# Optimization experiments

Measured on AMD Instinct MI355X. Metric: run time of the kernel, lower is better.

Reference implementation:

```python
import jax, jax.numpy as jnp
import numpy as np

D = 2048
N = 4096
HEAD = 2
DH = D // HEAD


def setup_inputs() -> dict:
    key = jax.random.key(0)
    ks = jax.random.split(key, 7)
    s = 0.02  # realistic init scale for weights
    x = jax.random.normal(ks[0], (1, N, D), jnp.float32)
    Wq1 = jax.random.normal(ks[1], (DH, DH), jnp.float32) * s
    Wq2 = jax.random.normal(ks[2], (DH, DH), jnp.float32) * s
    Wk1 = jax.random.normal(ks[3], (DH, DH), jnp.float32) * s
    Wk2 = jax.random.normal(ks[4], (DH, DH), jnp.float32) * s
    Wv1 = jax.random.normal(ks[5], (DH, DH), jnp.float32) * s
    Wv2 = jax.random.normal(ks[6], (DH, DH), jnp.float32) * s
    return {"x": x, "Wq1": Wq1, "Wq2": Wq2, "Wk1": Wk1, "Wk2": Wk2,
            "Wv1": Wv1, "Wv2": Wv2}


def _head(xh, Wq, Wk, Wv):
    # xh: [1, N, Dh]; Linear applies in @ W^T (no bias)
    q = (xh @ Wq.T)[0]                      # [N, Dh]
    k = (xh @ Wk.T)[0]                      # [N, Dh] (k reshaped to 2D in torch)
    v = (xh @ Wv.T)[0]                      # [N, Dh]
    # QK_T linear with weight dynamically set to k (detached in torch):
    Sc = q @ jax.lax.stop_gradient(k).T     # [N, N]
    # Sc_V linear on v^T with weight set to Sc (detached in torch):
    Sc = jax.lax.stop_gradient(Sc)
    return v.T @ Sc.T                       # [Dh, N]  == (Sc @ v)^T


def reference(x, Wq1, Wq2, Wk1, Wk2, Wv1, Wv2):
    Dh = Wq1.shape[0]
    x1, x2 = x[..., :Dh], x[..., Dh:]       # torch.chunk(x, 2, dim=2)
    o1 = _head(x1, Wq1, Wk1, Wv1)           # [Dh, N]
    o2 = _head(x2, Wq2, Wk2, Wv2)           # [Dh, N]
    out = jnp.concatenate([o1, o2], axis=0).T  # transpose(-2,-1).squeeze -> [N, D]
    return out
```

## Files before the change

kernel.cpp:

```cpp
#include <hip/hip_runtime.h>
#include <hip/hip_bf16.h>


using bf16 = __hip_bfloat16;
typedef __attribute__((ext_vector_type(8))) __bf16 bf16x8;
typedef __attribute__((ext_vector_type(8))) unsigned short u16x8;
typedef __attribute__((ext_vector_type(4))) float f32x4;

#define M1 (1024 * 1024)

struct GB {
    const bf16* A[8];
    const bf16* B[8];
    void*       C[8];
    int lda[8];
    int ldb[8];
};

__device__ __forceinline__ void gload_lds16(const void* g, void* l) {
    __builtin_amdgcn_global_load_lds(
        (const __attribute__((address_space(1))) void*)g,
        (__attribute__((address_space(3))) void*)l, 16, 0, 0);
}

__device__ __forceinline__ void waitv0() {
    asm volatile("s_waitcnt vmcnt(0)" ::: "memory");
}

template<int BM_, int BN_, typename OUT_T>
__device__ __forceinline__ void gemm_core(
    const bf16* __restrict__ A, int lda,
    const bf16* __restrict__ B, int ldb,
    OUT_T* __restrict__ C, int ldc,
    int m0, int n0, int Ksub,
    unsigned short* smem, int tid)
{
    constexpr int BK = 64;
    unsigned short* As = smem;
    unsigned short* Bs = smem + BM_ * BK;

    constexpr int MI = BM_ / 32;
    constexpr int NI = BN_ / 32;

    const int lane = tid & 63;
    const int wave = tid >> 6;
    const int wm   = wave >> 1;
    const int wn   = wave & 1;
    const int fr = lane & 15;
    const int kg = lane >> 4;

    const int srow  = tid >> 3;
    const int scol  = (tid & 7) * 8;
    const int scolg = scol ^ ((srow & 7) << 3);

    f32x4 acc[MI][NI];
    #pragma unroll
    for (int i = 0; i < MI; ++i)
        #pragma unroll
        for (int j = 0; j < NI; ++j)
            acc[i][j] = {0.f, 0.f, 0.f, 0.f};

    const int niter = Ksub >> 6;
    for (int it = 0; it < niter; ++it) {
        const int kt = it << 6;
        #pragma unroll
        for (int r = 0; r < BM_ / 32; ++r)
            gload_lds16(A + (size_t)(m0 + r * 32 + srow) * lda + (kt + scolg),
                        &As[(r * 32 + srow) * BK + scol]);
        #pragma unroll
        for (int r = 0; r < BN_ / 32; ++r)
            gload_lds16(B + (size_t)(n0 + r * 32 + srow) * ldb + (kt + scolg),
                        &Bs[(r * 32 + srow) * BK + scol]);
        waitv0();
        __builtin_amdgcn_s_barrier();
        __builtin_amdgcn_sched_barrier(0);

        #pragma unroll
        for (int kk = 0; kk < 2; ++kk) {
            bf16x8 af[MI], bfg[NI];
            #pragma unroll
            for (int mi = 0; mi < MI; ++mi) {
                const int row = wm * (BM_ / 2) + mi * 16 + fr;
                const int c = (kk * 32 + kg * 8) ^ ((row & 7) << 3);
                af[mi] = *(const bf16x8*)&As[row * BK + c];
            }
            #pragma unroll
            for (int ni = 0; ni < NI; ++ni) {
                const int row = wn * (BN_ / 2) + ni * 16 + fr;
                const int c = (kk * 32 + kg * 8) ^ ((row & 7) << 3);
                bfg[ni] = *(const bf16x8*)&Bs[row * BK + c];
            }
            #pragma unroll
            for (int mi = 0; mi < MI; ++mi)
                #pragma unroll
                for (int ni = 0; ni < NI; ++ni)
                    acc[mi][ni] = __builtin_amdgcn_mfma_f32_16x16x32_bf16(
                        af[mi], bfg[ni], acc[mi][ni], 0, 0, 0);
        }

        __builtin_amdgcn_sched_barrier(0);
        __builtin_amdgcn_s_barrier();
        __builtin_amdgcn_sched_barrier(0);
    }

    if constexpr (sizeof(OUT_T) == 2) {
        #pragma unroll
        for (int mi = 0; mi < MI; ++mi)
            #pragma unroll
            for (int ni = 0; ni < NI; ++ni) {
                const int c = wn * (BN_ / 2) + ni * 16 + fr;
                #pragma unroll
                for (int j = 0; j < 4; ++j) {
                    const int r = wm * (BM_ / 2) + mi * 16 + kg * 4 + j;
                    bf16 h = __float2bfloat16(acc[mi][ni][j]);
                    smem[r * BN_ + c] = *(unsigned short*)&h;
                }
            }
        __syncthreads();
        constexpr int V = (BM_ * BN_) / 2048;
        #pragma unroll
        for (int v = 0; v < V; ++v) {
            const int off = v * 2048 + tid * 8;
            const int r = off / BN_;
            const int c = off % BN_;
            *(u16x8*)((unsigned short*)C + (size_t)(m0 + r) * ldc + n0 + c) =
                *(const u16x8*)&smem[off];
        }
    } else {
        float* fs = (float*)smem;
        #pragma unroll
        for (int mi = 0; mi < MI; ++mi)
            #pragma unroll
            for (int ni = 0; ni < NI; ++ni) {
                const int c = wn * (BN_ / 2) + ni * 16 + fr;
                #pragma unroll
                for (int j = 0; j < 4; ++j) {
                    const int r = wm * (BM_ / 2) + mi * 16 + kg * 4 + j;
                    fs[r * BN_ + c] = acc[mi][ni][j];
                }
            }
        __syncthreads();
        constexpr int V = (BM_ * BN_) / 1024;
        #pragma unroll
        for (int v = 0; v < V; ++v) {
            const int off = v * 1024 + tid * 4;
            const int r = off / BN_;
            const int c = off % BN_;
            *(float4*)((float*)C + (size_t)(m0 + r) * ldc + n0 + c) =
                *(const float4*)&fs[off];
        }
    }
}

template<int BM_, int BN_, typename OUT_T>
__global__ __launch_bounds__(256, 4)
void gemm_bt_pa(GB g, int Ksub, int ldc)
{
    constexpr int STAGE_SH = (BM_ + BN_) * 64;
    constexpr int EPI_SH   = BM_ * BN_ * (int)sizeof(OUT_T) / 2;
    constexpr int SMEM_SH  = STAGE_SH > EPI_SH ? STAGE_SH : EPI_SH;
    __shared__ __align__(16) unsigned short smem[SMEM_SH];

    const int gx = gridDim.x, gy = gridDim.y;
    const int nwg = gx * gy * gridDim.z;
    const int orig = blockIdx.x + gx * (blockIdx.y + gy * blockIdx.z);
    const int cpx = nwg >> 3;
    const int wg = (orig & 7) * cpx + (orig >> 3);
    const int bx = wg % gx;
    const int by = (wg / gx) % gy;
    const int bz = wg / (gx * gy);

    gemm_core<BM_, BN_, OUT_T>(g.A[bz], g.lda[bz], g.B[bz], g.ldb[bz],
                               (OUT_T*)g.C[bz], ldc,
                               by * BM_, bx * BN_, Ksub,
                               smem, threadIdx.x);
}

struct B1Args {
    const bf16* xt;
    const bf16* wdst;
    bf16* Gp;
    bf16* Mb;
};

__global__ __launch_bounds__(256, 4)
void b1_kernel(B1Args a)
{
    __shared__ __align__(16) unsigned short smem[16384];

    const int nwg = 704;
    const int orig = blockIdx.x;
    const int cpx = nwg >> 3;
    const int wg = (orig & 7) * cpx + (orig >> 3);

    if (wg < 576) {
        const int z = wg / 36;
        const int tile = wg - z * 36;
        const int h = z >> 3, s = z & 7;
        int ti = 0, rem = tile;
        while (rem >= 8 - ti) { rem -= 8 - ti; ++ti; }
        const int tj = ti + rem;
        const bf16* A = a.xt + (size_t)(h * 1024 + ti * 128) * 4096 + s * 512;
        const bf16* B = a.xt + (size_t)(h * 1024 + tj * 128) * 4096 + s * 512;
        bf16* C = a.Gp + ((size_t)z * 36 + tile) * 16384;
        gemm_core<128, 128, bf16>(A, 4096, B, 4096, C, 128, 0, 0, 512,
                                  smem, threadIdx.x);
    } else {
        const int idx = wg - 576;
        const int h = idx >> 6;
        const int tile = idx & 63;
        const int m0 = (tile >> 3) * 128;
        const int n0 = (tile & 7) * 128;
        const bf16* A = a.wdst + (size_t)h * M1;
        const bf16* B = a.wdst + (size_t)(2 + h) * M1;
        bf16* C = a.Mb + (size_t)h * M1;
        gemm_core<128, 128, bf16>(A, 1024, B, 1024, C, 1024, m0, n0, 1024,
                                  smem, threadIdx.x);
    }
}


__device__ __forceinline__ ushort4 cvt4(float4 v) {
    ushort4 o; bf16 h;
    h = __float2bfloat16(v.x); o.x = *(unsigned short*)&h;
    h = __float2bfloat16(v.y); o.y = *(unsigned short*)&h;
    h = __float2bfloat16(v.z); o.z = *(unsigned short*)&h;
    h = __float2bfloat16(v.w); o.w = *(unsigned short*)&h;
    return o;
}

struct PrepArgs {
    const float* x;
    const float* w[4];
    const float* wv[2];
    bf16* xb;
    bf16* xt;
    bf16* wdst;
};

__device__ void xpose64(const float* __restrict__ src, int ldsrc,
                        int r0, int c0,
                        bf16* __restrict__ dstS, int ldS,
                        bf16* __restrict__ dstT, int ldT,
                        float (*tile)[65], int t)
{
    const int tr  = t >> 4;
    const int tc4 = (t & 15) * 4;
    #pragma unroll
    for (int ph = 0; ph < 4; ++ph) {
        const int row = ph * 16 + tr;
        float4 v = *(const float4*)(src + (size_t)(r0 + row) * ldsrc + c0 + tc4);
        tile[row][tc4 + 0] = v.x;
        tile[row][tc4 + 1] = v.y;
        tile[row][tc4 + 2] = v.z;
        tile[row][tc4 + 3] = v.w;
        if (dstS)
            *(ushort4*)((unsigned short*)dstS + (size_t)(r0 + row) * ldS + c0 + tc4) = cvt4(v);
    }
    __syncthreads();
    #pragma unroll
    for (int ph = 0; ph < 4; ++ph) {
        const int crow = ph * 16 + tr;
        float4 v = {tile[tc4 + 0][crow], tile[tc4 + 1][crow],
                    tile[tc4 + 2][crow], tile[tc4 + 3][crow]};
        *(ushort4*)((unsigned short*)dstT + (size_t)(c0 + crow) * ldT + r0 + tc4) = cvt4(v);
    }
}

__global__ void prep(PrepArgs p)
{
    __shared__ float tile[64][65];
    const int b = blockIdx.x;
    const int t = threadIdx.x;

    if (b < 2048) {
        const int n0 = (b & 63) * 64;
        const int c0 = (b >> 6) * 64;
        xpose64(p.x, 2048, n0, c0, p.xb, 2048, p.xt, 4096, tile, t);
    } else if (b < 3072) {
        const int i = b - 2048;
        const int mat = i >> 8;
        const int tl  = i & 255;
        const int r0 = (tl & 15) * 64;
        const int c0 = (tl >> 4) * 64;
        xpose64(p.w[mat], 1024, r0, c0, nullptr, 0,
                p.wdst + (size_t)mat * M1, 1024, tile, t);
    } else {
        const int i = b - 3072;
        const int mat = i >> 9;
        const int blk = i & 511;
        const size_t off = (size_t)blk * 2048 + t * 8;
        float4 v0 = *(const float4*)(p.wv[mat] + off);
        float4 v1 = *(const float4*)(p.wv[mat] + off + 4);
        unsigned short* d = (unsigned short*)p.wdst + (size_t)(4 + mat) * M1 + off;
        *(ushort4*)d       = cvt4(v0);
        *(ushort4*)(d + 4) = cvt4(v1);
    }
}


__device__ __forceinline__ void reduce_slices(const unsigned short* src,
                                              unsigned short* dst,
                                              int h, int r, int nslice)
{
    float acc[8] = {0, 0, 0, 0, 0, 0, 0, 0};
    for (int s = 0; s < nslice; ++s) {
        u16x8 v = *(const u16x8*)(src + ((size_t)(h * nslice + s) << 20) + r);
        #pragma unroll
        for (int j = 0; j < 8; ++j)
            acc[j] += __uint_as_float(((unsigned)v[j]) << 16);
    }
    u16x8 o;
    #pragma unroll
    for (int j = 0; j < 8; ++j) {
        bf16 hh = __float2bfloat16(acc[j]);
        o[j] = *(unsigned short*)&hh;
    }
    *(u16x8*)(dst + ((size_t)h << 20) + r) = o;
}

__global__ void reduce_G(const unsigned short* Gp, unsigned short* Gd)
{
    const int b = blockIdx.x, t = threadIdx.x;
    const int h    = b / 288;
    const int rem  = b - h * 288;
    const int tile = rem >> 3;
    const int blk  = rem & 7;
    int ti = 0, trem = tile;
    while (trem >= 8 - ti) { trem -= 8 - ti; ++ti; }
    const int tj = ti + trem;

    const int e  = blk * 2048 + t * 8;
    const int r  = e >> 7;
    const int c0 = e & 127;

    float acc[8] = {0, 0, 0, 0, 0, 0, 0, 0};
    for (int s = 0; s < 8; ++s) {
        u16x8 v = *(const u16x8*)(Gp + ((size_t)(h * 8 + s) * 36 + tile) * 16384 + e);
        #pragma unroll
        for (int j = 0; j < 8; ++j)
            acc[j] += __uint_as_float(((unsigned)v[j]) << 16);
    }
    u16x8 o;
    #pragma unroll
    for (int j = 0; j < 8; ++j) {
        bf16 hh = __float2bfloat16(acc[j]);
        o[j] = *(unsigned short*)&hh;
    }
    unsigned short* G = Gd + (size_t)h * M1;
    *(u16x8*)(G + (size_t)(ti * 128 + r) * 1024 + tj * 128 + c0) = o;
    if (ti != tj) {
        #pragma unroll
        for (int j = 0; j < 8; ++j)
            G[(size_t)(tj * 128 + c0 + j) * 1024 + ti * 128 + r] = o[j];
    }
}

__global__ void reduce_4(const unsigned short* Sp, unsigned short* Dd)
{
    const int e = (blockIdx.x * 256 + threadIdx.x) * 8;
    reduce_slices(Sp, Dd, e >> 20, e & (M1 - 1), 4);
}


extern "C" void kernel_launch(void* const* d_in, const int* in_sizes, int n_in,
                              void* d_out, int out_size, void* d_ws, size_t ws_size,
                              hipStream_t stream)
{
    bf16* xb   = (bf16*)d_ws;
    bf16* xt   = xb + 8 * M1;
    bf16* wdst = xt + 8 * M1;
    bf16* Mb   = wdst + 6 * M1;
    bf16* Gb   = Mb + 2 * M1;
    bf16* Ytb  = Gb + 2 * M1;
    bf16* Utb  = Ytb + 2 * M1;

    bf16* scr = (bf16*)d_out;

    PrepArgs pa;
    pa.x = (const float*)d_in[0];
    pa.w[0] = (const float*)d_in[1];  pa.w[1] = (const float*)d_in[2];
    pa.w[2] = (const float*)d_in[3];  pa.w[3] = (const float*)d_in[4];
    pa.wv[0] = (const float*)d_in[5]; pa.wv[1] = (const float*)d_in[6];
    pa.xb = xb; pa.xt = xt; pa.wdst = wdst;
    prep<<<4096, 256, 0, stream>>>(pa);

    B1Args b1;
    b1.xt = xt; b1.wdst = wdst; b1.Gp = scr; b1.Mb = Mb;
    b1_kernel<<<704, 256, 0, stream>>>(b1);

    reduce_G<<<576, 256, 0, stream>>>((const unsigned short*)scr,
                                      (unsigned short*)Gb);

    GB g;

    for (int z = 0; z < 8; ++z) {
        const int h = z >> 2, s = z & 3;
        g.A[z] = Mb + (size_t)h * M1 + s * 256;  g.lda[z] = 1024;
        g.B[z] = Gb + (size_t)h * M1 + s * 256;  g.ldb[z] = 1024;
        g.C[z] = (bf16*)scr + (size_t)z * M1;
    }
    gemm_bt_pa<128, 128, bf16><<<dim3(8, 8, 8), 256, 0, stream>>>(g, 256, 1024);

    reduce_4<<<1024, 256, 0, stream>>>((const unsigned short*)scr, (unsigned short*)Ytb);

    for (int z = 0; z < 8; ++z) {
        const int h = z >> 2, s = z & 3;
        g.A[z] = wdst + (size_t)(4 + h) * M1 + s * 256;  g.lda[z] = 1024;
        g.B[z] = Ytb + (size_t)h * M1 + s * 256;         g.ldb[z] = 1024;
        g.C[z] = (bf16*)scr + (size_t)z * M1;
    }
    gemm_bt_pa<128, 128, bf16><<<dim3(8, 8, 8), 256, 0, stream>>>(g, 256, 1024);

    reduce_4<<<1024, 256, 0, stream>>>((const unsigned short*)scr, (unsigned short*)Utb);

    for (int z = 0; z < 2; ++z) {
        g.A[z] = xb + (size_t)z * 1024;   g.lda[z] = 2048;
        g.B[z] = Utb + (size_t)z * M1;    g.ldb[z] = 1024;
        g.C[z] = (float*)d_out + (size_t)z * 1024;
    }
    gemm_bt_pa<128, 64, float><<<dim3(16, 32, 2), 256, 0, stream>>>(g, 1024, 2048);
}
```

Baseline: 115.3 us.

## Reassociate attention chain to N-side GEMMs and fuse Gram reduction with Q projection

Changes the matrix-product association. The old version chained small 1024x1024 products (M·G, then Wv·Y), each split-K into scratch with its own reduce kernel, before one final N-sized GEMM. The new version computes Q' = x·Mt per head, R = Q'·G, and out = R·Wv^T as three N x 1024 x 1024 GEMMs, and fuses the Gram-matrix slice reduction into the same launch as the Q' projection. This removes two split-K reduce passes and several launches. In exchange it does more FLOPs on N-length operands and adds 16M elements of bf16 intermediate traffic, with an extra rounding to bf16 at an intermediate stage.

```diff
diff --git a/kernel.cpp b/kernel.cpp
--- a/kernel.cpp
+++ b/kernel.cpp
@@ -180,7 +180,7 @@
     const bf16* xt;
     const bf16* wdst;
     bf16* Gp;
-    bf16* Mb;
+    bf16* Mtb;
 };
 
 __global__ __launch_bounds__(256, 4)
@@ -211,11 +211,76 @@
         const int tile = idx & 63;
         const int m0 = (tile >> 3) * 128;
         const int n0 = (tile & 7) * 128;
-        const bf16* A = a.wdst + (size_t)h * M1;
-        const bf16* B = a.wdst + (size_t)(2 + h) * M1;
-        bf16* C = a.Mb + (size_t)h * M1;
+        const bf16* A = a.wdst + (size_t)(2 + h) * M1;
+        const bf16* B = a.wdst + (size_t)h * M1;
+        bf16* C = a.Mtb + (size_t)h * M1;
         gemm_core<128, 128, bf16>(A, 1024, B, 1024, C, 1024, m0, n0, 1024,
                                   smem, threadIdx.x);
+    }
+}
+
+struct QRArgs {
+    const bf16* xb;
+    const bf16* Mtb;
+    const unsigned short* Gp;
+    bf16* Qp;
+    unsigned short* Gd;
+};
+
+__global__ __launch_bounds__(256, 4)
+void q_redg_kernel(QRArgs a)
+{
+    __shared__ __align__(16) unsigned short smem[12288];
+
+    const int nwg = 1600;
+    const int orig = blockIdx.x;
+    const int cpx = nwg >> 3;
+    const int wg = (orig & 7) * cpx + (orig >> 3);
+
+    if (wg < 1024) {
+        const int bx = wg & 15;
+        const int by = (wg >> 4) & 31;
+        const int h  = wg >> 9;
+        gemm_core<128, 64, bf16>(a.xb + h * 1024, 2048,
+                                 a.Mtb + (size_t)h * M1, 1024,
+                                 a.Qp + (size_t)h * 4 * M1, 1024,
+                                 by * 128, bx * 64, 1024,
+                                 smem, threadIdx.x);
+    } else {
+        const int b = wg - 1024;
+        const int t = threadIdx.x;
+        const int h    = b / 288;
+        const int rem  = b - h * 288;
+        const int tile = rem >> 3;
+        const int blk  = rem & 7;
+        int ti = 0, trem = tile;
+        while (trem >= 8 - ti) { trem -= 8 - ti; ++ti; }
+        const int tj = ti + trem;
+
+        const int e  = blk * 2048 + t * 8;
+        const int r  = e >> 7;
+        const int c0 = e & 127;
+
+        float acc[8] = {0, 0, 0, 0, 0, 0, 0, 0};
+        for (int s = 0; s < 8; ++s) {
+            u16x8 v = *(const u16x8*)(a.Gp + ((size_t)(h * 8 + s) * 36 + tile) * 16384 + e);
+            #pragma unroll
+            for (int j = 0; j < 8; ++j)
+                acc[j] += __uint_as_float(((unsigned)v[j]) << 16);
+        }
+        u16x8 o;
+        #pragma unroll
+        for (int j = 0; j < 8; ++j) {
+            bf16 hh = __float2bfloat16(acc[j]);
+            o[j] = *(unsigned short*)&hh;
+        }
+        unsigned short* G = a.Gd + (size_t)h * M1;
+        *(u16x8*)(G + (size_t)(ti * 128 + r) * 1024 + tj * 128 + c0) = o;
+        if (ti != tj) {
+            #pragma unroll
+            for (int j = 0; j < 8; ++j)
+                G[(size_t)(tj * 128 + c0 + j) * 1024 + ti * 128 + r] = o[j];
+        }
     }
 }
 
@@ -299,70 +364,6 @@
 }
 
 
-__device__ __forceinline__ void reduce_slices(const unsigned short* src,
-                                              unsigned short* dst,
-                                              int h, int r, int nslice)
-{
-    float acc[8] = {0, 0, 0, 0, 0, 0, 0, 0};
-    for (int s = 0; s < nslice; ++s) {
-        u16x8 v = *(const u16x8*)(src + ((size_t)(h * nslice + s) << 20) + r);
-        #pragma unroll
-        for (int j = 0; j < 8; ++j)
-            acc[j] += __uint_as_float(((unsigned)v[j]) << 16);
-    }
-    u16x8 o;
-    #pragma unroll
-    for (int j = 0; j < 8; ++j) {
-        bf16 hh = __float2bfloat16(acc[j]);
-        o[j] = *(unsigned short*)&hh;
-    }
-    *(u16x8*)(dst + ((size_t)h << 20) + r) = o;
-}
-
-__global__ void reduce_G(const unsigned short* Gp, unsigned short* Gd)
-{
-    const int b = blockIdx.x, t = threadIdx.x;
-    const int h    = b / 288;
-    const int rem  = b - h * 288;
-    const int tile = rem >> 3;
-    const int blk  = rem & 7;
-    int ti = 0, trem = tile;
-    while (trem >= 8 - ti) { trem -= 8 - ti; ++ti; }
-    const int tj = ti + trem;
-
-    const int e  = blk * 2048 + t * 8;
-    const int r  = e >> 7;
-    const int c0 = e & 127;
-
-    float acc[8] = {0, 0, 0, 0, 0, 0, 0, 0};
-    for (int s = 0; s < 8; ++s) {
-        u16x8 v = *(const u16x8*)(Gp + ((size_t)(h * 8 + s) * 36 + tile) * 16384 + e);
-        #pragma unroll
-        for (int j = 0; j < 8; ++j)
-            acc[j] += __uint_as_float(((unsigned)v[j]) << 16);
-    }
-    u16x8 o;
-    #pragma unroll
-    for (int j = 0; j < 8; ++j) {
-        bf16 hh = __float2bfloat16(acc[j]);
-        o[j] = *(unsigned short*)&hh;
-    }
-    unsigned short* G = Gd + (size_t)h * M1;
-    *(u16x8*)(G + (size_t)(ti * 128 + r) * 1024 + tj * 128 + c0) = o;
-    if (ti != tj) {
-        #pragma unroll
-        for (int j = 0; j < 8; ++j)
-            G[(size_t)(tj * 128 + c0 + j) * 1024 + ti * 128 + r] = o[j];
-    }
-}
-
-__global__ void reduce_4(const unsigned short* Sp, unsigned short* Dd)
-{
-    const int e = (blockIdx.x * 256 + threadIdx.x) * 8;
-    reduce_slices(Sp, Dd, e >> 20, e & (M1 - 1), 4);
-}
-
-
 extern "C" void kernel_launch(void* const* d_in, const int* in_sizes, int n_in,
                               void* d_out, int out_size, void* d_ws, size_t ws_size,
                               hipStream_t stream)
@@ -370,10 +371,10 @@
     bf16* xb   = (bf16*)d_ws;
     bf16* xt   = xb + 8 * M1;
     bf16* wdst = xt + 8 * M1;
-    bf16* Mb   = wdst + 6 * M1;
-    bf16* Gb   = Mb + 2 * M1;
-    bf16* Ytb  = Gb + 2 * M1;
-    bf16* Utb  = Ytb + 2 * M1;
+    bf16* Mtb  = wdst + 6 * M1;
+    bf16* Gb   = Mtb + 2 * M1;
+    bf16* Qp   = Gb + 2 * M1;
+    bf16* Rb   = Qp + 8 * M1;
 
     bf16* scr = (bf16*)d_out;
 
@@ -386,37 +387,26 @@
     prep<<<4096, 256, 0, stream>>>(pa);
 
     B1Args b1;
-    b1.xt = xt; b1.wdst = wdst; b1.Gp = scr; b1.Mb = Mb;
+    b1.xt = xt; b1.wdst = wdst; b1.Gp = scr; b1.Mtb = Mtb;
     b1_kernel<<<704, 256, 0, stream>>>(b1);
 
-    reduce_G<<<576, 256, 0, stream>>>((const unsigned short*)scr,
-                                      (unsigned short*)Gb);
+    QRArgs qr;
+    qr.xb = xb; qr.Mtb = Mtb; qr.Gp = (const unsigned short*)scr;
+    qr.Qp = Qp; qr.Gd = (unsigned short*)Gb;
+    q_redg_kernel<<<1600, 256, 0, stream>>>(qr);
 
     GB g;
 
-    for (int z = 0; z < 8; ++z) {
-        const int h = z >> 2, s = z & 3;
-        g.A[z] = Mb + (size_t)h * M1 + s * 256;  g.lda[z] = 1024;
-        g.B[z] = Gb + (size_t)h * M1 + s * 256;  g.ldb[z] = 1024;
-        g.C[z] = (bf16*)scr + (size_t)z * M1;
-    }
-    gemm_bt_pa<128, 128, bf16><<<dim3(8, 8, 8), 256, 0, stream>>>(g, 256, 1024);
-
-    reduce_4<<<1024, 256, 0, stream>>>((const unsigned short*)scr, (unsigned short*)Ytb);
-
-    for (int z = 0; z < 8; ++z) {
-        const int h = z >> 2, s = z & 3;
-        g.A[z] = wdst + (size_t)(4 + h) * M1 + s * 256;  g.lda[z] = 1024;
-        g.B[z] = Ytb + (size_t)h * M1 + s * 256;         g.ldb[z] = 1024;
-        g.C[z] = (bf16*)scr + (size_t)z * M1;
-    }
-    gemm_bt_pa<128, 128, bf16><<<dim3(8, 8, 8), 256, 0, stream>>>(g, 256, 1024);
-
-    reduce_4<<<1024, 256, 0, stream>>>((const unsigned short*)scr, (unsigned short*)Utb);
-
     for (int z = 0; z < 2; ++z) {
-        g.A[z] = xb + (size_t)z * 1024;   g.lda[z] = 2048;
-        g.B[z] = Utb + (size_t)z * M1;    g.ldb[z] = 1024;
+        g.A[z] = Qp + (size_t)z * 4 * M1;  g.lda[z] = 1024;
+        g.B[z] = Gb + (size_t)z * M1;      g.ldb[z] = 1024;
+        g.C[z] = Rb + (size_t)z * 4 * M1;
+    }
+    gemm_bt_pa<128, 64, bf16><<<dim3(16, 32, 2), 256, 0, stream>>>(g, 1024, 1024);
+
+    for (int z = 0; z < 2; ++z) {
+        g.A[z] = Rb + (size_t)z * 4 * M1;           g.lda[z] = 1024;
+        g.B[z] = wdst + (size_t)(4 + z) * M1;       g.ldb[z] = 1024;
         g.C[z] = (float*)d_out + (size_t)z * 1024;
     }
     gemm_bt_pa<128, 64, float><<<dim3(16, 32, 2), 256, 0, stream>>>(g, 1024, 2048);
```

After: 130.5 us. 1.13x slower.
